# Optimization experiments

Hardware: AMD Instinct MI355X
Metric: run time of the kernel (lower is better)

The kernel has to match this reference:

```python
import jax, jax.numpy as jnp
import numpy as np

N, E = 100000, 3200000
F_IN, C1, C2, H, NC = 256, 32, 64, 128, 10


def _winit(key, shape, scale=0.05):
    return scale * jax.random.normal(key, shape, jnp.float32)


def setup_inputs() -> dict:
    key = jax.random.key(0)
    ks = jax.random.split(key, 20)
    inp = {
        "x": jax.random.normal(ks[0], (N, F_IN), jnp.float32),
        "edge_index": jax.random.randint(ks[1], (2, E), 0, N, jnp.int32),
        "edge_attr": jax.random.uniform(ks[2], (E, 1), jnp.float32),
        # conv1 (LEConv in->32): lin1 (W,b), lin2 (W, no bias), lin3 (W,b)
        "W1a": _winit(ks[3], (F_IN, C1)), "b1a": jnp.zeros((C1,), jnp.float32),
        "W1b": _winit(ks[4], (F_IN, C1)),
        "W1c": _winit(ks[5], (F_IN, C1)), "b1c": jnp.zeros((C1,), jnp.float32),
        # conv2 (LEConv 32->64)
        "W2a": _winit(ks[6], (C1, C2)), "b2a": jnp.zeros((C2,), jnp.float32),
        "W2b": _winit(ks[7], (C1, C2)),
        "W2c": _winit(ks[8], (C1, C2)), "b2c": jnp.zeros((C2,), jnp.float32),
        # fc layers
        "Wf1": _winit(ks[9], (C2, H)), "bf1": jnp.zeros((H,), jnp.float32),
        "Wf2": _winit(ks[10], (H, NC)), "bf2": jnp.zeros((NC,), jnp.float32),
    }
    return inp


def _leconv(x, src, dst, ew, Wa, ba, Wb, Wc, bc):
    # PyG LEConv: x'_i = sum_{j->i} e_ji * (lin1(x)_j - lin2(x)_i) + lin3(x)_i
    a = x @ Wa + ba           # [N, C]
    b = x @ Wb                # [N, C] (no bias)
    msg = ew[:, None] * (a[src] - b[dst])  # [E, C]
    agg = jax.ops.segment_sum(msg, dst, num_segments=x.shape[0])
    return agg + x @ Wc + bc


def reference(x, edge_index, edge_attr,
              W1a, b1a, W1b, W1c, b1c,
              W2a, b2a, W2b, W2c, b2c,
              Wf1, bf1, Wf2, bf2):
    src, dst = edge_index[0], edge_index[1]
    ew = edge_attr.squeeze(-1)
    h = jax.nn.elu(_leconv(x, src, dst, ew, W1a, b1a, W1b, W1c, b1c))
    h = jax.nn.elu(_leconv(h, src, dst, ew, W2a, b2a, W2b, W2c, b2c))
    h = jax.nn.elu(h @ Wf1 + bf1)
    logits = h @ Wf2 + bf2
    return jax.nn.log_softmax(logits, axis=1)
```

## Files before the change

kernel.cpp:

```cpp
#include <hip/hip_runtime.h>
#include <cmath>

#define N_NODES 100000
#define E_EDGES 3200000
#define CAP 80
#define NPB 512
#define NB  196
#define BKT_CAP 17408
#define ST2_T 1024

typedef float f4v __attribute__((ext_vector_type(4)));

__device__ __forceinline__ float elu_f(float x) { return x > 0.0f ? x : expm1f(x); }

__device__ __forceinline__ unsigned short f2bf(float f) {
    unsigned int u = __float_as_uint(f);
    u += 0x7FFFu + ((u >> 16) & 1u);
    return (unsigned short)(u >> 16);
}
__device__ __forceinline__ float bf_lo(unsigned int u) { return __uint_as_float(u << 16); }
__device__ __forceinline__ float bf_hi(unsigned int u) { return __uint_as_float(u & 0xFFFF0000u); }

__device__ __forceinline__ unsigned int f2fp8(float f) {
    return (unsigned int)(__builtin_amdgcn_cvt_pk_fp8_f32(f, 0.f, 0, false)) & 0xFFu;
}
#define FMA8(W, VX, VY) do { \
    acc[0] = fmaf((W), __builtin_amdgcn_cvt_f32_fp8((VX), 0), acc[0]); \
    acc[1] = fmaf((W), __builtin_amdgcn_cvt_f32_fp8((VX), 1), acc[1]); \
    acc[2] = fmaf((W), __builtin_amdgcn_cvt_f32_fp8((VX), 2), acc[2]); \
    acc[3] = fmaf((W), __builtin_amdgcn_cvt_f32_fp8((VX), 3), acc[3]); \
    acc[4] = fmaf((W), __builtin_amdgcn_cvt_f32_fp8((VY), 0), acc[4]); \
    acc[5] = fmaf((W), __builtin_amdgcn_cvt_f32_fp8((VY), 1), acc[5]); \
    acc[6] = fmaf((W), __builtin_amdgcn_cvt_f32_fp8((VY), 2), acc[6]); \
    acc[7] = fmaf((W), __builtin_amdgcn_cvt_f32_fp8((VY), 3), acc[7]); \
} while (0)

__global__ __launch_bounds__(256) void zero_kernel(float* __restrict__ p, int n) {
    int i = blockIdx.x * 256 + threadIdx.x;
    if (i < n) p[i] = 0.0f;
}
__global__ __launch_bounds__(256) void iota_cap(unsigned int* __restrict__ off) {
    int i = blockIdx.x * 256 + threadIdx.x;
    if (i < N_NODES) off[i] = (unsigned int)i * CAP;
}

__global__ __launch_bounds__(256) void k1_bucket(
    const int* __restrict__ ei, const float* __restrict__ ew,
    unsigned int* __restrict__ btail, unsigned long long* __restrict__ bkt,
    const float* __restrict__ x,
    const float* __restrict__ W1a, const float* __restrict__ b1a,
    const float* __restrict__ W1b,
    const float* __restrict__ W1c, const float* __restrict__ b1c,
    unsigned char* __restrict__ a1f, float* __restrict__ pre1, float* __restrict__ br1)
{
    __shared__ unsigned int shm[8192];
    const int tid = threadIdx.x;
    const int b = blockIdx.x;
    const int g = b / 3, r = b - 3 * g;
    if (r == 0) {
        unsigned int* lcnt  = shm;
        unsigned int* gbase = shm + 256;
        lcnt[tid] = 0u;
        __syncthreads();
        const int e0 = g * 2048 + tid;
        int d[8]; unsigned int pay[8], slot[8]; bool ok[8];
#pragma unroll
        for (int k = 0; k < 8; ++k) {
            int e = e0 + 256 * k;
            ok[k] = (e < E_EDGES);
            int ee = ok[k] ? e : 0;
            d[k] = __builtin_nontemporal_load(ei + E_EDGES + ee);
            int s = __builtin_nontemporal_load(ei + ee);
            float w = __builtin_nontemporal_load(ew + ee);
            unsigned int q = (unsigned int)(w * 32768.0f);
            if (q > 32767u) q = 32767u;
            pay[k] = ((unsigned int)s << 15) | q;
        }
#pragma unroll
        for (int k = 0; k < 8; ++k)
            if (ok[k]) slot[k] = atomicAdd(&lcnt[d[k] >> 9], 1u);
        __syncthreads();
        unsigned int c = lcnt[tid];
        if (tid < NB && c > 0u) gbase[tid] = atomicAdd(&btail[tid], c);
        __syncthreads();
#pragma unroll
        for (int k = 0; k < 8; ++k) {
            if (!ok[k]) continue;
            int bin = d[k] >> 9;
            unsigned int pos = gbase[bin] + slot[k];
            if (pos < BKT_CAP)
                bkt[(size_t)bin * BKT_CAP + pos] =
                    ((unsigned long long)(unsigned int)d[k] << 32) | (unsigned long long)pay[k];
        }
        return;
    }
    const int t = 2 * g + (r - 1);
    if (t >= N_NODES / 32) return;
    float* xs = (float*)shm;
    const int n0 = t * 32;
    for (int i = tid * 4; i < 8192; i += 1024) {
        f4v tv = __builtin_nontemporal_load((const f4v*)(x + (size_t)n0 * 256 + i));
        *(f4v*)(xs + i) = tv;
    }
    __syncthreads();

    const int c = tid & 31;
    const int grp = tid >> 5;
    float aa[4], ab[4], ac[4];
#pragma unroll
    for (int j = 0; j < 4; ++j) { aa[j] = 0.f; ab[j] = 0.f; ac[j] = 0.f; }

#pragma unroll 4
    for (int k4 = 0; k4 < 64; ++k4) {
        f4v xv[4];
#pragma unroll
        for (int j = 0; j < 4; ++j)
            xv[j] = *(const f4v*)(xs + (grp + 8 * j) * 256 + 4 * k4);
#pragma unroll
        for (int i = 0; i < 4; ++i) {
            int wi = (4 * k4 + i) * 32 + c;
            float wa = W1a[wi], wb = W1b[wi], wc = W1c[wi];
#pragma unroll
            for (int j = 0; j < 4; ++j) {
                float xvv = xv[j][i];
                aa[j] = fmaf(xvv, wa, aa[j]);
                ab[j] = fmaf(xvv, wb, ab[j]);
                ac[j] = fmaf(xvv, wc, ac[j]);
            }
        }
    }
#pragma unroll
    for (int j = 0; j < 4; ++j) {
        int n = n0 + grp + 8 * j;
        __builtin_nontemporal_store((unsigned char)f2fp8(aa[j] + b1a[c]), a1f + (size_t)n * 32 + c);
        __builtin_nontemporal_store(ac[j] + b1c[c], pre1 + (size_t)n * 32 + c);
        __builtin_nontemporal_store(ab[j], br1 + (size_t)n * 32 + c);
    }
}

__global__ __launch_bounds__(ST2_T) void scatter2(
    const unsigned int* __restrict__ btail, const unsigned long long* __restrict__ bkt,
    unsigned int* __restrict__ cnt, float* __restrict__ wsum,
    unsigned int* __restrict__ off, unsigned int* __restrict__ rec)
{
    __shared__ unsigned int c0[512];
    __shared__ unsigned int sa[512];
    __shared__ unsigned int sb[512];
    __shared__ float swsum[512];
    const int bin = blockIdx.x;
    const int tid = threadIdx.x;
    unsigned int nrec = btail[bin];
    if (nrec > BKT_CAP) nrec = BKT_CAP;
    const unsigned long long* bb = bkt + (size_t)bin * BKT_CAP;
    const unsigned int n0b = (unsigned int)bin * NPB;
    for (int i = tid; i < 512; i += ST2_T) { c0[i] = 0u; swsum[i] = 0.f; }
    __syncthreads();
    for (unsigned int i = tid; i < nrec; i += ST2_T) {
        unsigned long long rcd = __builtin_nontemporal_load(bb + i);
        unsigned int pay = (unsigned int)rcd;
        unsigned int ln = (unsigned int)(rcd >> 32) - n0b;
        atomicAdd(&c0[ln], 1u);
        atomicAdd(&swsum[ln], (float)(pay & 32767u) * (1.0f / 32768.0f));
    }
    __syncthreads();
    for (int i = tid; i < 512; i += ST2_T) sa[i] = c0[i];
    __syncthreads();
    unsigned int* src = sa; unsigned int* dst = sb;
    for (int step = 1; step < 512; step <<= 1) {
        for (int i = tid; i < 512; i += ST2_T)
            dst[i] = src[i] + ((i >= step) ? src[i - step] : 0u);
        __syncthreads();
        unsigned int* t = src; src = dst; dst = t;
    }
    for (int i = tid; i < 512; i += ST2_T) dst[i] = src[i] - c0[i];
    __syncthreads();
    for (int i = tid; i < 512; i += ST2_T) c0[i] = 0u;
    __syncthreads();
    const unsigned int bkt_base = (unsigned int)bin * BKT_CAP;
    for (unsigned int i = tid; i < nrec; i += ST2_T) {
        unsigned long long rcd = __builtin_nontemporal_load(bb + i);
        unsigned int pay = (unsigned int)rcd;
        unsigned int ln = (unsigned int)(rcd >> 32) - n0b;
        unsigned int idx = atomicAdd(&c0[ln], 1u);
        rec[bkt_base + dst[ln] + idx] = pay;
    }
    __syncthreads();
    for (int i = tid; i < 512; i += ST2_T) {
        unsigned int n = n0b + (unsigned int)i;
        if (n < N_NODES) {
            cnt[n]  = c0[i];
            wsum[n] = swsum[i];
            off[n]  = bkt_base + dst[i];
        }
    }
}

__global__ __launch_bounds__(256) void k1_direct(
    const int* __restrict__ ei, const float* __restrict__ ew,
    unsigned int* __restrict__ cnt, float* __restrict__ wsum,
    unsigned int* __restrict__ rec,
    const float* __restrict__ x,
    const float* __restrict__ W1a, const float* __restrict__ b1a,
    const float* __restrict__ W1b,
    const float* __restrict__ W1c, const float* __restrict__ b1c,
    unsigned char* __restrict__ a1f, float* __restrict__ pre1, float* __restrict__ br1)
{
    __shared__ float xs[32 * 256];
    const int tid = threadIdx.x;
    const int b = blockIdx.x;
    if ((b & 1) == 0) {
        const int e0 = (b >> 1) * 1024 + tid;
        int d[4], s[4]; float w[4];
#pragma unroll
        for (int k = 0; k < 4; ++k) {
            d[k] = __builtin_nontemporal_load(ei + E_EDGES + e0 + 256 * k);
            s[k] = __builtin_nontemporal_load(ei + e0 + 256 * k);
            w[k] = __builtin_nontemporal_load(ew + e0 + 256 * k);
        }
#pragma unroll
        for (int k = 0; k < 4; ++k) unsafeAtomicAdd(&wsum[d[k]], w[k]);
        unsigned int idx[4];
#pragma unroll
        for (int k = 0; k < 4; ++k) idx[k] = atomicAdd(&cnt[d[k]], 1u);
#pragma unroll
        for (int k = 0; k < 4; ++k) {
            unsigned int kk = idx[k];
            if (kk > CAP - 1) kk = CAP - 1;
            unsigned int q = (unsigned int)(w[k] * 32768.0f);
            if (q > 32767u) q = 32767u;
            rec[(size_t)d[k] * CAP + kk] = ((unsigned int)s[k] << 15) | q;
        }
        return;
    }
    const int n0 = (b >> 1) * 32;
    for (int i = tid * 4; i < 8192; i += 1024) {
        f4v t = __builtin_nontemporal_load((const f4v*)(x + (size_t)n0 * 256 + i));
        *(f4v*)(xs + i) = t;
    }
    __syncthreads();
    const int c = tid & 31;
    const int grp = tid >> 5;
    float aa[4], ab[4], ac[4];
#pragma unroll
    for (int j = 0; j < 4; ++j) { aa[j] = 0.f; ab[j] = 0.f; ac[j] = 0.f; }
#pragma unroll 4
    for (int k4 = 0; k4 < 64; ++k4) {
        f4v xv[4];
#pragma unroll
        for (int j = 0; j < 4; ++j)
            xv[j] = *(const f4v*)(xs + (grp + 8 * j) * 256 + 4 * k4);
#pragma unroll
        for (int i = 0; i < 4; ++i) {
            int wi = (4 * k4 + i) * 32 + c;
            float wa = W1a[wi], wb = W1b[wi], wc = W1c[wi];
#pragma unroll
            for (int j = 0; j < 4; ++j) {
                float xvv = xv[j][i];
                aa[j] = fmaf(xvv, wa, aa[j]);
                ab[j] = fmaf(xvv, wb, ab[j]);
                ac[j] = fmaf(xvv, wc, ac[j]);
            }
        }
    }
#pragma unroll
    for (int j = 0; j < 4; ++j) {
        int n = n0 + grp + 8 * j;
        __builtin_nontemporal_store((unsigned char)f2fp8(aa[j] + b1a[c]), a1f + (size_t)n * 32 + c);
        __builtin_nontemporal_store(ac[j] + b1c[c], pre1 + (size_t)n * 32 + c);
        __builtin_nontemporal_store(ab[j], br1 + (size_t)n * 32 + c);
    }
}

__global__ __launch_bounds__(256) void gather1(const unsigned int* __restrict__ cnt,
                                               const float* __restrict__ wsum,
                                               const unsigned int* __restrict__ off,
                                               const unsigned int* __restrict__ rec,
                                               const uint2* __restrict__ a2,
                                               const float* __restrict__ pre1,
                                               const float* __restrict__ br1,
                                               uint4* __restrict__ h4,
                                               uint2* __restrict__ h2f)
{
    const int sub = threadIdx.x & 3;
    const int n = blockIdx.x * 64 + (threadIdx.x >> 2);
    if (n >= N_NODES) return;
    int deg = (int)cnt[n];
    if (deg > CAP) deg = CAP;
    const float ws = wsum[n];
    const unsigned int* rrow = rec + off[n];
    float acc[8];
#pragma unroll
    for (int i = 0; i < 8; ++i) acc[i] = 0.f;
    int j = 0;
    for (; j + 4 <= deg; j += 4) {
        unsigned int r0 = rrow[j], r1 = rrow[j + 1], r2 = rrow[j + 2], r3 = rrow[j + 3];
        float w0 = (float)(r0 & 32767u) * (1.0f / 32768.0f);
        float w1 = (float)(r1 & 32767u) * (1.0f / 32768.0f);
        float w2 = (float)(r2 & 32767u) * (1.0f / 32768.0f);
        float w3 = (float)(r3 & 32767u) * (1.0f / 32768.0f);
        uint2 v0 = a2[(size_t)(r0 >> 15) * 4 + sub];
        uint2 v1 = a2[(size_t)(r1 >> 15) * 4 + sub];
        uint2 v2 = a2[(size_t)(r2 >> 15) * 4 + sub];
        uint2 v3 = a2[(size_t)(r3 >> 15) * 4 + sub];
        FMA8(w0, v0.x, v0.y);
        FMA8(w1, v1.x, v1.y);
        FMA8(w2, v2.x, v2.y);
        FMA8(w3, v3.x, v3.y);
    }
    for (; j < deg; ++j) {
        unsigned int r0 = rrow[j];
        float w0 = (float)(r0 & 32767u) * (1.0f / 32768.0f);
        uint2 v0 = a2[(size_t)(r0 >> 15) * 4 + sub];
        FMA8(w0, v0.x, v0.y);
    }
    const float* pp = pre1 + (size_t)n * 32 + sub * 8;
    const float* bp = br1 + (size_t)n * 32 + sub * 8;
    float4 p0 = *(const float4*)pp, p1 = *(const float4*)(pp + 4);
    float4 q0 = *(const float4*)bp, q1 = *(const float4*)(bp + 4);
    float e0 = elu_f(p0.x + acc[0] - ws * q0.x);
    float e1 = elu_f(p0.y + acc[1] - ws * q0.y);
    float e2 = elu_f(p0.z + acc[2] - ws * q0.z);
    float e3 = elu_f(p0.w + acc[3] - ws * q0.w);
    float e4 = elu_f(p1.x + acc[4] - ws * q1.x);
    float e5 = elu_f(p1.y + acc[5] - ws * q1.y);
    float e6 = elu_f(p1.z + acc[6] - ws * q1.z);
    float e7 = elu_f(p1.w + acc[7] - ws * q1.w);
    uint4 o;
    o.x = (unsigned int)f2bf(e0) | ((unsigned int)f2bf(e1) << 16);
    o.y = (unsigned int)f2bf(e2) | ((unsigned int)f2bf(e3) << 16);
    o.z = (unsigned int)f2bf(e4) | ((unsigned int)f2bf(e5) << 16);
    o.w = (unsigned int)f2bf(e6) | ((unsigned int)f2bf(e7) << 16);
    h4[(size_t)n * 4 + sub] = o;
    int w0 = __builtin_amdgcn_cvt_pk_fp8_f32(e0, e1, 0, false);
    w0 = __builtin_amdgcn_cvt_pk_fp8_f32(e2, e3, w0, true);
    int w1 = __builtin_amdgcn_cvt_pk_fp8_f32(e4, e5, 0, false);
    w1 = __builtin_amdgcn_cvt_pk_fp8_f32(e6, e7, w1, true);
    h2f[(size_t)n * 4 + sub] = make_uint2((unsigned int)w0, (unsigned int)w1);
}

__global__ __launch_bounds__(256) void tail_kernel(
    const unsigned int* __restrict__ cnt,
    const float* __restrict__ wsum,
    const unsigned int* __restrict__ off,
    const unsigned int* __restrict__ rec,
    const unsigned int* __restrict__ h1h,
    const uint2* __restrict__ h1f,
    const float* __restrict__ W2a, const float* __restrict__ b2a,
    const float* __restrict__ W2b,
    const float* __restrict__ W2c, const float* __restrict__ b2c,
    const float* __restrict__ Wf1, const float* __restrict__ bf1,
    const float* __restrict__ Wf2, const float* __restrict__ bf2,
    float* __restrict__ out)
{
    __shared__ float smem[6144];
    float* g2s = smem;
    float* hs  = smem + 2048;
    float* asp = smem + 3072;
    float* ts  = smem + 2048;
    __shared__ float b2sh[10];
    __shared__ float wsn[32];

    const int tid = threadIdx.x;
    const int n0 = blockIdx.x * 32;
    if (tid < 10) b2sh[tid] = bf2[tid];
    for (int i = tid; i < 512; i += 256) {
        unsigned int u = h1h[(size_t)n0 * 16 + i];
        hs[2 * i]     = bf_lo(u);
        hs[2 * i + 1] = bf_hi(u);
    }
    {
        const int node = tid >> 3, sub = tid & 7;
        const int q = sub & 3, half = sub >> 2;
        const int n = n0 + node;
        int deg = (int)cnt[n];
        if (deg > CAP) deg = CAP;
        if (sub == 0) wsn[node] = wsum[n];
        const unsigned int* rrow = rec + off[n];
        float acc[8];
#pragma unroll
        for (int i = 0; i < 8; ++i) acc[i] = 0.f;
        int j = half;
        for (; j + 6 < deg; j += 8) {
            unsigned int r0 = rrow[j], r1 = rrow[j + 2], r2 = rrow[j + 4], r3 = rrow[j + 6];
            float w0 = (float)(r0 & 32767u) * (1.0f / 32768.0f);
            float w1 = (float)(r1 & 32767u) * (1.0f / 32768.0f);
            float w2 = (float)(r2 & 32767u) * (1.0f / 32768.0f);
            float w3 = (float)(r3 & 32767u) * (1.0f / 32768.0f);
            uint2 v0 = h1f[(size_t)(r0 >> 15) * 4 + q];
            uint2 v1 = h1f[(size_t)(r1 >> 15) * 4 + q];
            uint2 v2 = h1f[(size_t)(r2 >> 15) * 4 + q];
            uint2 v3 = h1f[(size_t)(r3 >> 15) * 4 + q];
            FMA8(w0, v0.x, v0.y);
            FMA8(w1, v1.x, v1.y);
            FMA8(w2, v2.x, v2.y);
            FMA8(w3, v3.x, v3.y);
        }
        for (; j < deg; j += 2) {
            unsigned int r0 = rrow[j];
            float w0 = (float)(r0 & 32767u) * (1.0f / 32768.0f);
            uint2 v0 = h1f[(size_t)(r0 >> 15) * 4 + q];
            FMA8(w0, v0.x, v0.y);
        }
        float* ap = asp + node * 64 + half * 32 + q * 8;
#pragma unroll
        for (int i = 0; i < 8; ++i) ap[i] = acc[i];
    }
    __syncthreads();

    const int c = tid & 31;
    const int grp = tid >> 5;
    {
        float Aa[4][2], Ab[4][2], Ac[4][2];
#pragma unroll
        for (int j = 0; j < 4; ++j)
#pragma unroll
            for (int cb = 0; cb < 2; ++cb) { Aa[j][cb] = 0.f; Ab[j][cb] = 0.f; Ac[j][cb] = 0.f; }
#pragma unroll 8
        for (int k = 0; k < 32; ++k) {
            float hv[4], av[4];
#pragma unroll
            for (int j = 0; j < 4; ++j) {
                int nd = grp + 8 * j;
                hv[j] = hs[nd * 32 + k];
                av[j] = asp[nd * 64 + k] + asp[nd * 64 + 32 + k];
            }
#pragma unroll
            for (int cb = 0; cb < 2; ++cb) {
                int wi = k * 64 + cb * 32 + c;
                float wa = W2a[wi], wb = W2b[wi], wc = W2c[wi];
#pragma unroll
                for (int j = 0; j < 4; ++j) {
                    Aa[j][cb] = fmaf(av[j], wa, Aa[j][cb]);
                    Ab[j][cb] = fmaf(hv[j], wb, Ab[j][cb]);
                    Ac[j][cb] = fmaf(hv[j], wc, Ac[j][cb]);
                }
            }
        }
        __syncthreads();
#pragma unroll
        for (int j = 0; j < 4; ++j) {
            float w = wsn[grp + 8 * j];
#pragma unroll
            for (int cb = 0; cb < 2; ++cb) {
                int col = cb * 32 + c;
                float g = Ac[j][cb] + b2c[col] + Aa[j][cb] + w * (b2a[col] - Ab[j][cb]);
                g2s[(grp + 8 * j) * 64 + col] = elu_f(g);
            }
        }
    }
    __syncthreads();
    {
        float acc2[4][4];
#pragma unroll
        for (int j = 0; j < 4; ++j)
#pragma unroll
            for (int cb = 0; cb < 4; ++cb) acc2[j][cb] = 0.f;
#pragma unroll 8
        for (int k = 0; k < 64; ++k) {
            float hv[4];
#pragma unroll
            for (int j = 0; j < 4; ++j) hv[j] = g2s[(grp + 8 * j) * 64 + k];
#pragma unroll
            for (int cb = 0; cb < 4; ++cb) {
                float wv = Wf1[k * 128 + cb * 32 + c];
#pragma unroll
                for (int j = 0; j < 4; ++j) acc2[j][cb] = fmaf(hv[j], wv, acc2[j][cb]);
            }
        }
#pragma unroll
        for (int j = 0; j < 4; ++j)
#pragma unroll
            for (int cb = 0; cb < 4; ++cb) {
                int col = cb * 32 + c;
                ts[(grp + 8 * j) * 128 + col] = elu_f(acc2[j][cb] + bf1[col]);
            }
    }
    __syncthreads();
    float* w2s = smem;
    for (int i = tid; i < 1280; i += 256) w2s[i] = Wf2[i];
    __syncthreads();
    {
        const int node = tid >> 3, sub = tid & 7;
        float p[10];
#pragma unroll
        for (int o = 0; o < 10; ++o) p[o] = 0.f;
        const float* trow = ts + node * 128;
#pragma unroll
        for (int kk = 0; kk < 16; ++kk) {
            int k = sub + 8 * kk;
            float tv = trow[k];
#pragma unroll
            for (int o = 0; o < 10; ++o) p[o] = fmaf(tv, w2s[k * 10 + o], p[o]);
        }
#pragma unroll
        for (int off2 = 4; off2 >= 1; off2 >>= 1) {
#pragma unroll
            for (int o = 0; o < 10; ++o) p[o] += __shfl_xor(p[o], off2, 64);
        }
        if (sub == 0) {
            float lg[10];
#pragma unroll
            for (int o = 0; o < 10; ++o) lg[o] = p[o] + b2sh[o];
            float m = lg[0];
#pragma unroll
            for (int o = 1; o < 10; ++o) m = fmaxf(m, lg[o]);
            float s = 0.f;
#pragma unroll
            for (int o = 0; o < 10; ++o) s += expf(lg[o] - m);
            float lse = m + logf(s);
#pragma unroll
            for (int o = 0; o < 10; ++o) out[(size_t)(n0 + node) * 10 + o] = lg[o] - lse;
        }
    }
}

extern "C" void kernel_launch(void* const* d_in, const int* in_sizes, int n_in,
                              void* d_out, int out_size, void* d_ws, size_t ws_size,
                              hipStream_t stream) {
    const float* x    = (const float*)d_in[0];
    const int*   ei   = (const int*)d_in[1];
    const float* ew   = (const float*)d_in[2];
    const float* W1a  = (const float*)d_in[3];
    const float* b1a  = (const float*)d_in[4];
    const float* W1b  = (const float*)d_in[5];
    const float* W1c  = (const float*)d_in[6];
    const float* b1c  = (const float*)d_in[7];
    const float* W2a  = (const float*)d_in[8];
    const float* b2a  = (const float*)d_in[9];
    const float* W2b  = (const float*)d_in[10];
    const float* W2c  = (const float*)d_in[11];
    const float* b2c  = (const float*)d_in[12];
    const float* Wf1  = (const float*)d_in[13];
    const float* bf1  = (const float*)d_in[14];
    const float* Wf2  = (const float*)d_in[15];
    const float* bf2  = (const float*)d_in[16];
    float* out = (float*)d_out;

    const size_t N = N_NODES;
    float* ws = (float*)d_ws;
    unsigned int*   cnt   = (unsigned int*)ws;
    float*          wsum  = ws + N;
    unsigned int*   off   = (unsigned int*)(ws + 2 * N);
    unsigned int*   btail = (unsigned int*)(ws + 3 * N);
    unsigned int*   rec   = (unsigned int*)(ws + 3 * N + 512);
    float*          A0    = ws + 3 * N + 512 + (size_t)CAP * N;
    unsigned char*  a1f   = (unsigned char*)A0;
    float*          pre1  = A0 + 8 * N;
    float*          br1   = A0 + 40 * N;
    unsigned int*   h1h   = (unsigned int*)(A0 + 72 * N);
    uint2*          h1f   = (uint2*)(A0 + 88 * N);
    unsigned long long* bkt = (unsigned long long*)(A0 + 96 * N);

    const size_t need_bytes = ((size_t)179 * N + 512 + (size_t)NB * BKT_CAP * 2) * 4;

    zero_kernel<<<(3 * N_NODES + 512 + 255) / 256, 256, 0, stream>>>(ws, 3 * N_NODES + 512);

    if (ws_size >= need_bytes) {
        k1_bucket<<<3 * 1563, 256, 0, stream>>>(
            ei, ew, btail, bkt, x, W1a, b1a, W1b, W1c, b1c, a1f, pre1, br1);
        scatter2<<<NB, ST2_T, 0, stream>>>(btail, bkt, cnt, wsum, off, rec);
    } else {
        iota_cap<<<(N_NODES + 255) / 256, 256, 0, stream>>>(off);
        k1_direct<<<2 * (N_NODES / 32), 256, 0, stream>>>(
            ei, ew, cnt, wsum, rec, x, W1a, b1a, W1b, W1c, b1c, a1f, pre1, br1);
    }

    gather1<<<(N_NODES + 63) / 64, 256, 0, stream>>>(
        cnt, wsum, off, rec, (const uint2*)a1f, pre1, br1, (uint4*)h1h, h1f);

    tail_kernel<<<N_NODES / 32, 256, 0, stream>>>(
        cnt, wsum, off, rec, h1h, h1f, W2a, b2a, W2b, W2c, b2c, Wf1, bf1, Wf2, bf2, out);
}
```

Before: 508.0 us.

## Fuse layer-1 gather into bucket scatter kernel and shrink zeroing

On the bucketed path, the layer-1 neighbour gather plus ELU and bf16/fp8 packing now runs inside the scatter kernel. It reuses the per-bin counts, weight sums and offsets already held in shared memory, and reads the just-written record rows while they are likely still in cache. This removes the separate gather1 launch and its reloads of cnt, wsum and off. The full workspace zeroing is replaced by a tiny kernel that clears only the bucket tails. The tradeoff is that the random-access gather now runs on only 196 blocks, so it may be limited by latency and occupancy compared with the previous grid of about 1.5k blocks.

Result: no change. 506.6 us (-0.3%).

```diff
diff --git a/kernel.cpp b/kernel.cpp
--- a/kernel.cpp
+++ b/kernel.cpp
@@ -38,6 +38,9 @@
 __global__ __launch_bounds__(256) void zero_kernel(float* __restrict__ p, int n) {
     int i = blockIdx.x * 256 + threadIdx.x;
     if (i < n) p[i] = 0.0f;
+}
+__global__ __launch_bounds__(256) void zero_btail(unsigned int* __restrict__ p) {
+    if (threadIdx.x < 512) p[threadIdx.x] = 0u;
 }
 __global__ __launch_bounds__(256) void iota_cap(unsigned int* __restrict__ off) {
     int i = blockIdx.x * 256 + threadIdx.x;
@@ -138,10 +141,15 @@
     }
 }
 
-__global__ __launch_bounds__(ST2_T) void scatter2(
+__global__ __launch_bounds__(ST2_T) void scatter2_fused(
     const unsigned int* __restrict__ btail, const unsigned long long* __restrict__ bkt,
     unsigned int* __restrict__ cnt, float* __restrict__ wsum,
-    unsigned int* __restrict__ off, unsigned int* __restrict__ rec)
+    unsigned int* __restrict__ off, unsigned int* __restrict__ rec,
+    const uint2* __restrict__ a2,
+    const float* __restrict__ pre1,
+    const float* __restrict__ br1,
+    uint4* __restrict__ h4,
+    uint2* __restrict__ h2f)
 {
     __shared__ unsigned int c0[512];
     __shared__ unsigned int sa[512];
@@ -192,6 +200,65 @@
             wsum[n] = swsum[i];
             off[n]  = bkt_base + dst[i];
         }
+    }
+#pragma unroll
+    for (int pass = 0; pass < 2; ++pass) {
+        const int ln = pass * 256 + (tid >> 2);
+        const int sub = tid & 3;
+        const unsigned int n = n0b + (unsigned int)ln;
+        if (n >= N_NODES) continue;
+        int deg = (int)c0[ln];
+        if (deg > CAP) deg = CAP;
+        const float wsv = swsum[ln];
+        const unsigned int* rrow = rec + bkt_base + dst[ln];
+        float acc[8];
+#pragma unroll
+        for (int i = 0; i < 8; ++i) acc[i] = 0.f;
+        int j = 0;
+        for (; j + 4 <= deg; j += 4) {
+            unsigned int r0 = rrow[j], r1 = rrow[j + 1], r2 = rrow[j + 2], r3 = rrow[j + 3];
+            float w0 = (float)(r0 & 32767u) * (1.0f / 32768.0f);
+            float w1 = (float)(r1 & 32767u) * (1.0f / 32768.0f);
+            float w2 = (float)(r2 & 32767u) * (1.0f / 32768.0f);
+            float w3 = (float)(r3 & 32767u) * (1.0f / 32768.0f);
+            uint2 v0 = a2[(size_t)(r0 >> 15) * 4 + sub];
+            uint2 v1 = a2[(size_t)(r1 >> 15) * 4 + sub];
+            uint2 v2 = a2[(size_t)(r2 >> 15) * 4 + sub];
+            uint2 v3 = a2[(size_t)(r3 >> 15) * 4 + sub];
+            FMA8(w0, v0.x, v0.y);
+            FMA8(w1, v1.x, v1.y);
+            FMA8(w2, v2.x, v2.y);
+            FMA8(w3, v3.x, v3.y);
+        }
+        for (; j < deg; ++j) {
+            unsigned int r0 = rrow[j];
+            float w0 = (float)(r0 & 32767u) * (1.0f / 32768.0f);
+            uint2 v0 = a2[(size_t)(r0 >> 15) * 4 + sub];
+            FMA8(w0, v0.x, v0.y);
+        }
+        const float* pp = pre1 + (size_t)n * 32 + sub * 8;
+        const float* bp = br1 + (size_t)n * 32 + sub * 8;
+        float4 p0 = *(const float4*)pp, p1 = *(const float4*)(pp + 4);
+        float4 q0 = *(const float4*)bp, q1 = *(const float4*)(bp + 4);
+        float e0 = elu_f(p0.x + acc[0] - wsv * q0.x);
+        float e1 = elu_f(p0.y + acc[1] - wsv * q0.y);
+        float e2 = elu_f(p0.z + acc[2] - wsv * q0.z);
+        float e3 = elu_f(p0.w + acc[3] - wsv * q0.w);
+        float e4 = elu_f(p1.x + acc[4] - wsv * q1.x);
+        float e5 = elu_f(p1.y + acc[5] - wsv * q1.y);
+        float e6 = elu_f(p1.z + acc[6] - wsv * q1.z);
+        float e7 = elu_f(p1.w + acc[7] - wsv * q1.w);
+        uint4 o;
+        o.x = (unsigned int)f2bf(e0) | ((unsigned int)f2bf(e1) << 16);
+        o.y = (unsigned int)f2bf(e2) | ((unsigned int)f2bf(e3) << 16);
+        o.z = (unsigned int)f2bf(e4) | ((unsigned int)f2bf(e5) << 16);
+        o.w = (unsigned int)f2bf(e6) | ((unsigned int)f2bf(e7) << 16);
+        h4[(size_t)n * 4 + sub] = o;
+        int w0p = __builtin_amdgcn_cvt_pk_fp8_f32(e0, e1, 0, false);
+        w0p = __builtin_amdgcn_cvt_pk_fp8_f32(e2, e3, w0p, true);
+        int w1p = __builtin_amdgcn_cvt_pk_fp8_f32(e4, e5, 0, false);
+        w1p = __builtin_amdgcn_cvt_pk_fp8_f32(e6, e7, w1p, true);
+        h2f[(size_t)n * 4 + sub] = make_uint2((unsigned int)w0p, (unsigned int)w1p);
     }
 }
 
@@ -286,7 +353,7 @@
     if (n >= N_NODES) return;
     int deg = (int)cnt[n];
     if (deg > CAP) deg = CAP;
-    const float ws = wsum[n];
+    const float wsv = wsum[n];
     const unsigned int* rrow = rec + off[n];
     float acc[8];
 #pragma unroll
@@ -317,25 +384,25 @@
     const float* bp = br1 + (size_t)n * 32 + sub * 8;
     float4 p0 = *(const float4*)pp, p1 = *(const float4*)(pp + 4);
     float4 q0 = *(const float4*)bp, q1 = *(const float4*)(bp + 4);
-    float e0 = elu_f(p0.x + acc[0] - ws * q0.x);
-    float e1 = elu_f(p0.y + acc[1] - ws * q0.y);
-    float e2 = elu_f(p0.z + acc[2] - ws * q0.z);
-    float e3 = elu_f(p0.w + acc[3] - ws * q0.w);
-    float e4 = elu_f(p1.x + acc[4] - ws * q1.x);
-    float e5 = elu_f(p1.y + acc[5] - ws * q1.y);
-    float e6 = elu_f(p1.z + acc[6] - ws * q1.z);
-    float e7 = elu_f(p1.w + acc[7] - ws * q1.w);
+    float e0 = elu_f(p0.x + acc[0] - wsv * q0.x);
+    float e1 = elu_f(p0.y + acc[1] - wsv * q0.y);
+    float e2 = elu_f(p0.z + acc[2] - wsv * q0.z);
+    float e3 = elu_f(p0.w + acc[3] - wsv * q0.w);
+    float e4 = elu_f(p1.x + acc[4] - wsv * q1.x);
+    float e5 = elu_f(p1.y + acc[5] - wsv * q1.y);
+    float e6 = elu_f(p1.z + acc[6] - wsv * q1.z);
+    float e7 = elu_f(p1.w + acc[7] - wsv * q1.w);
     uint4 o;
     o.x = (unsigned int)f2bf(e0) | ((unsigned int)f2bf(e1) << 16);
     o.y = (unsigned int)f2bf(e2) | ((unsigned int)f2bf(e3) << 16);
     o.z = (unsigned int)f2bf(e4) | ((unsigned int)f2bf(e5) << 16);
     o.w = (unsigned int)f2bf(e6) | ((unsigned int)f2bf(e7) << 16);
     h4[(size_t)n * 4 + sub] = o;
-    int w0 = __builtin_amdgcn_cvt_pk_fp8_f32(e0, e1, 0, false);
-    w0 = __builtin_amdgcn_cvt_pk_fp8_f32(e2, e3, w0, true);
-    int w1 = __builtin_amdgcn_cvt_pk_fp8_f32(e4, e5, 0, false);
-    w1 = __builtin_amdgcn_cvt_pk_fp8_f32(e6, e7, w1, true);
-    h2f[(size_t)n * 4 + sub] = make_uint2((unsigned int)w0, (unsigned int)w1);
+    int w0p = __builtin_amdgcn_cvt_pk_fp8_f32(e0, e1, 0, false);
+    w0p = __builtin_amdgcn_cvt_pk_fp8_f32(e2, e3, w0p, true);
+    int w1p = __builtin_amdgcn_cvt_pk_fp8_f32(e4, e5, 0, false);
+    w1p = __builtin_amdgcn_cvt_pk_fp8_f32(e6, e7, w1p, true);
+    h2f[(size_t)n * 4 + sub] = make_uint2((unsigned int)w0p, (unsigned int)w1p);
 }
 
 __global__ __launch_bounds__(256) void tail_kernel(
@@ -553,20 +620,21 @@
 
     const size_t need_bytes = ((size_t)179 * N + 512 + (size_t)NB * BKT_CAP * 2) * 4;
 
-    zero_kernel<<<(3 * N_NODES + 512 + 255) / 256, 256, 0, stream>>>(ws, 3 * N_NODES + 512);
-
     if (ws_size >= need_bytes) {
+        zero_btail<<<2, 256, 0, stream>>>(btail);
         k1_bucket<<<3 * 1563, 256, 0, stream>>>(
             ei, ew, btail, bkt, x, W1a, b1a, W1b, W1c, b1c, a1f, pre1, br1);
-        scatter2<<<NB, ST2_T, 0, stream>>>(btail, bkt, cnt, wsum, off, rec);
+        scatter2_fused<<<NB, ST2_T, 0, stream>>>(
+            btail, bkt, cnt, wsum, off, rec,
+            (const uint2*)a1f, pre1, br1, (uint4*)h1h, h1f);
     } else {
+        zero_kernel<<<(3 * N_NODES + 512 + 255) / 256, 256, 0, stream>>>(ws, 3 * N_NODES + 512);
         iota_cap<<<(N_NODES + 255) / 256, 256, 0, stream>>>(off);
         k1_direct<<<2 * (N_NODES / 32), 256, 0, stream>>>(
             ei, ew, cnt, wsum, rec, x, W1a, b1a, W1b, W1c, b1c, a1f, pre1, br1);
-    }
-
-    gather1<<<(N_NODES + 63) / 64, 256, 0, stream>>>(
-        cnt, wsum, off, rec, (const uint2*)a1f, pre1, br1, (uint4*)h1h, h1f);
+        gather1<<<(N_NODES + 63) / 64, 256, 0, stream>>>(
+            cnt, wsum, off, rec, (const uint2*)a1f, pre1, br1, (uint4*)h1h, h1f);
+    }
 
     tail_kernel<<<N_NODES / 32, 256, 0, stream>>>(
         cnt, wsum, off, rec, h1h, h1f, W2a, b2a, W2b, W2c, b2c, Wf1, bf1, Wf2, bf2, out);
```
